# Performance work log

Hardware: AMD Instinct MI355X
Metric: run time of the kernel (lower is better)

Reference implementation:

```python
import jax, jax.numpy as jnp
import numpy as np

C = 256  # in_channels
B, N = 8, 2048


def setup_inputs() -> dict:
    key = jax.random.key(0)
    ks = jax.random.split(key, 9)
    s = 1.0 / np.sqrt(C)  # conv1d default init scale (approx)
    return {
        "x": jax.random.normal(ks[0], (B, C, N), jnp.float32),
        "wq": jax.random.normal(ks[1], (C, C), jnp.float32) * s,
        "bq": jax.random.normal(ks[2], (C,), jnp.float32) * s,
        "wk": jax.random.normal(ks[3], (C, C), jnp.float32) * s,
        "bk": jax.random.normal(ks[4], (C,), jnp.float32) * s,
        "wv": jax.random.normal(ks[5], (C, C), jnp.float32) * s,
        "bv": jax.random.normal(ks[6], (C,), jnp.float32) * s,
        "wo": jax.random.normal(ks[7], (C, C), jnp.float32) * s,
        "bo": jax.random.normal(ks[8], (C,), jnp.float32) * s,
    }


def reference(x, wq, bq, wk, bk, wv, bv, wo, bo):
    # 1x1 Conv1d == channel-wise linear: [C_out,C_in] x [B,C_in,N] -> [B,C_out,N]
    proj = lambda w, b, t: jnp.einsum('ci,bin->bcn', w, t) + b[None, :, None]
    q = proj(wq, bq, x)
    k = proj(wk, bk, x)
    v = proj(wv, bv, x)
    norm = 1.0 / (x.shape[1] ** 0.5)
    # scores: w[b,n,m] = sum_c q[b,c,n] k[b,c,m]
    w = jnp.einsum('bcn,bcm->bnm', q, k) * norm
    w = jax.nn.softmax(w, axis=2)
    # attn output: sum_m v[b,c,m] w[b,n,m] -> [B,C,N]
    av = jnp.einsum('bcm,bnm->bcn', v, w)
    out = proj(wo, bo, av)
    return x + out
```

## Files before the change

kernel.cpp:

```cpp
#include <hip/hip_runtime.h>
#include <hip/hip_bf16.h>

#define CCH 256
#define NSEQ 2048
#define BATCH 8

typedef __hip_bfloat16 bf16;
typedef short s8v __attribute__((ext_vector_type(8)));
typedef float f4v __attribute__((ext_vector_type(4)));
typedef float f16v __attribute__((ext_vector_type(16)));

struct __align__(8) bf16x4 { bf16 v[4]; };

__device__ __forceinline__ float b2f(bf16 h) { return __bfloat162float(h); }
__device__ __forceinline__ bf16 f2b(float f) { return __float2bfloat16(f); }

#define MFMA16(a, b, c) __builtin_amdgcn_mfma_f32_16x16x32_bf16((a), (b), (c), 0, 0, 0)
#define MFMA32(a, b, c) __builtin_amdgcn_mfma_f32_32x32x16_bf16((a), (b), (c), 0, 0, 0)

__device__ __forceinline__ void gload_lds16(const bf16* g, bf16* l) {
    __builtin_amdgcn_global_load_lds(
        (const __attribute__((address_space(1))) unsigned int*)(g),
        (__attribute__((address_space(3))) unsigned int*)(l), 16, 0, 0);
}

__global__ __launch_bounds__(256) void prepw_kernel(
    const float* __restrict__ wq, const float* __restrict__ wk,
    const float* __restrict__ wv,
    bf16* __restrict__ wqb, bf16* __restrict__ wkb, bf16* __restrict__ wvb)
{
    int base = (blockIdx.x * 256 + threadIdx.x) * 8;
    int mat = base >> 16, off = base & 65535;
    const float* s = (mat == 0) ? wq : (mat == 1) ? wk : wv;
    bf16* d       = (mat == 0) ? wqb : (mat == 1) ? wkb : wvb;
    int doff = off ^ (((off >> 8) & 7) << 3);
    bf16 tmp[8];
    #pragma unroll
    for (int j = 0; j < 8; ++j) tmp[j] = f2b(s[off + j]);
    *(s8v*)&d[doff] = *(const s8v*)tmp;
}

__global__ __launch_bounds__(512, 4) void qkvprep_kernel(
    const float* __restrict__ x,
    const bf16* __restrict__ Wq, const bf16* __restrict__ Wk,
    const bf16* __restrict__ Wv,
    const float* __restrict__ bq, const float* __restrict__ bk,
    const float* __restrict__ bv,
    bf16* __restrict__ qTt, bf16* __restrict__ kTt, bf16* __restrict__ Vt)
{
    __shared__ bf16 xs[64][260];
    __shared__ bf16 wbuf[2][2][4096];

    const int tile = blockIdx.x;
    const int flat0 = tile * 64;
    const int phase = blockIdx.y;
    const int b = flat0 >> 11, nn = flat0 & 2047;
    const int tid = threadIdx.x;
    const int w = tid >> 6, lane = tid & 63;
    const int l15 = lane & 15, quad = lane >> 4;
    const int ng = w & 3;
    const int ch = w >> 2;
    const float* xb = x + (size_t)b * CCH * NSEQ;

    bf16* qt = qTt + (size_t)tile * 16384;
    bf16* kt = kTt + (size_t)tile * 16384;
    bf16* Vtb = Vt + (size_t)b * CCH * NSEQ;

    auto chunk_ptr = [&](int j) -> const bf16* {
        if (phase == 0)
            return (j < 8) ? Wq + (size_t)(ch * 8 + j) * 4096
                           : Wk + (size_t)(ch * 4 + (j - 8)) * 4096;
        else
            return (j < 8) ? Wv + (size_t)(ch * 8 + j) * 4096
                           : Wk + (size_t)(8 + ch * 4 + (j - 8)) * 4096;
    };
    auto stage = [&](int j, int par) {
        const bf16* src = chunk_ptr(j);
        bf16* dst = &wbuf[ch][par][0];
        int seg = (w & 3) * 2;
        gload_lds16(src + (seg + 0) * 512 + lane * 8, dst + (seg + 0) * 512);
        gload_lds16(src + (seg + 1) * 512 + lane * 8, dst + (seg + 1) * 512);
    };

    stage(0, 0);
    #pragma unroll
    for (int i = 0; i < 8; ++i) {
        int f4i = i * 512 + tid;
        int c = f4i >> 4, nq = f4i & 15;
        float4 v4 = *(const float4*)&xb[(size_t)c * NSEQ + nn + nq * 4];
        xs[nq * 4 + 0][c] = f2b(v4.x);
        xs[nq * 4 + 1][c] = f2b(v4.y);
        xs[nq * 4 + 2][c] = f2b(v4.z);
        xs[nq * 4 + 3][c] = f2b(v4.w);
    }
    __syncthreads();

    s8v xf[8];
    #pragma unroll
    for (int t = 0; t < 8; ++t)
        xf[t] = *(const s8v*)&xs[ng * 16 + l15][t * 32 + quad * 8];

    int par = 0;
    #pragma unroll
    for (int j = 0; j < 12; ++j) {
        if (j < 11) stage(j + 1, par ^ 1);

        const char* wb = (const char*)&wbuf[ch][par][0];
        s8v wf[8];
        #pragma unroll
        for (int t = 0; t < 8; ++t)
            wf[t] = *(const s8v*)(wb + l15 * 512 +
                                  ((t * 64 + quad * 16) ^ ((l15 & 7) << 4)));

        if (phase == 0 || j >= 8) {
            f4v a0 = {}, a1 = {};
            #pragma unroll
            for (int t = 0; t < 4; ++t) {
                a0 = MFMA16(wf[t], xf[t], a0);
                a1 = MFMA16(wf[t + 4], xf[t + 4], a1);
            }
            const bool isq = (phase == 0) && (j < 8);
            const int cs = (phase == 0)
                ? (j < 8 ? ch * 8 + j : ch * 4 + (j - 8))
                : (8 + ch * 4 + (j - 8));
            const float* bm = isq ? bq : bk;
            bf16* ot = isq ? qt : kt;
            const float sc = isq ? 0.0625f : 1.0f;
            float4 bb4 = *(const float4*)&bm[cs * 16 + quad * 4];
            float bbr[4] = { bb4.x, bb4.y, bb4.z, bb4.w };
            bf16x4 pk;
            #pragma unroll
            for (int r = 0; r < 4; ++r)
                pk.v[r] = f2b((a0[r] + a1[r] + bbr[r]) * sc);
            int nl = ng * 16 + l15;
            *(bf16x4*)&ot[(cs * 2 + (quad >> 1)) * 512 + nl * 8 + (quad & 1) * 4] = pk;
        } else {
            f4v a0 = {}, a1 = {};
            #pragma unroll
            for (int t = 0; t < 4; ++t) {
                a0 = MFMA16(xf[t], wf[t], a0);
                a1 = MFMA16(xf[t + 4], wf[t + 4], a1);
            }
            const int cs = ch * 8 + j;
            int c = cs * 16 + l15;
            float bb = bv[c];
            int nb0 = nn + ng * 16 + quad * 4;
            bf16x4 pk;
            #pragma unroll
            for (int r = 0; r < 4; ++r)
                pk.v[r] = f2b(a0[r] + a1[r] + bb);
            *(bf16x4*)&Vtb[(size_t)(nb0 >> 5) * 8192 + (size_t)c * 32 + (nb0 & 31)] = pk;
        }
        __syncthreads();
        par ^= 1;
    }
}

__global__ __launch_bounds__(256, 2) void flash_kernel(
    const bf16* __restrict__ qTt, const bf16* __restrict__ kTt,
    const bf16* __restrict__ Vt, bf16* __restrict__ Opart,
    float* __restrict__ lpart)
{
    __shared__ bf16 Kc[16384];
    __shared__ bf16 Ps[64][68];
    __shared__ float l_s[2][64];

    const int b = blockIdx.x, nt = blockIdx.y, ms = blockIdx.z;
    const int tid = threadIdx.x;
    const int W = tid >> 6, lane = tid & 63;
    const int l31 = lane & 31, h = lane >> 5;
    const int ng = W >> 1, mg = W & 1;
    const int mb = ms * 16;
    const bf16* Vtb = Vt + (size_t)b * CCH * NSEQ;

    s8v qf[16];
    {
        const bf16* qt = qTt + (size_t)(b * 32 + nt) * 16384;
        #pragma unroll
        for (int t = 0; t < 16; ++t)
            qf[t] = *(const s8v*)&qt[(t * 2 + h) * 512 + (ng * 32 + l31) * 8];
    }
    const bf16* vrow[2];
    #pragma unroll
    for (int cr = 0; cr < 2; ++cr)
        vrow[cr] = Vtb + (size_t)(W * 64 + cr * 32 + l31) * 32 + h * 8;

    f16v O[2][2] = {};
    float lacc[16] = {};

    {
        const bf16* kt = kTt + (size_t)(b * 32 + mb) * 16384;
        #pragma unroll
        for (int i = 0; i < 8; ++i) {
            int ch = W * 8 + i;
            gload_lds16(kt + ch * 512 + lane * 8, &Kc[ch * 512]);
        }
    }
    __syncthreads();

    for (int mt = 0; mt < 16; ++mt) {
        f16v S0 = {}, S1 = {};
        #pragma unroll
        for (int t = 0; t < 8; ++t) {
            s8v kf0 = *(const s8v*)&Kc[(t * 2 + h) * 512 + (mg * 32 + l31) * 8];
            s8v kf1 = *(const s8v*)&Kc[((t + 8) * 2 + h) * 512 + (mg * 32 + l31) * 8];
            S0 = MFMA32(qf[t], kf0, S0);
            S1 = MFMA32(qf[t + 8], kf1, S1);
        }
        s8v vf[2][4];
        #pragma unroll
        for (int ks = 0; ks < 4; ++ks)
            #pragma unroll
            for (int cr = 0; cr < 2; ++cr)
                vf[cr][ks] = *(const s8v*)(vrow[cr]
                    + (size_t)((mb + mt) * 2 + (ks >> 1)) * 8192
                    + (ks & 1) * 16);
        #pragma unroll
        for (int reg = 0; reg < 16; ++reg) {
            float e = __expf(fminf(S0[reg] + S1[reg], 60.f));
            lacc[reg] += e;
            int row = (reg & 3) + 8 * (reg >> 2) + 4 * h;
            Ps[ng * 32 + row][mg * 32 + l31] = f2b(e);
        }
        __syncthreads();

        if (mt < 15) {
            const bf16* kt = kTt + (size_t)(b * 32 + mb + mt + 1) * 16384;
            #pragma unroll
            for (int i = 0; i < 8; ++i) {
                int ch = W * 8 + i;
                gload_lds16(kt + ch * 512 + lane * 8, &Kc[ch * 512]);
            }
        }
        #pragma unroll
        for (int ks = 0; ks < 4; ++ks) {
            s8v pf0 = *(const s8v*)&Ps[l31][ks * 16 + h * 8];
            s8v pf1 = *(const s8v*)&Ps[32 + l31][ks * 16 + h * 8];
            O[0][0] = MFMA32(vf[0][ks], pf0, O[0][0]);
            O[0][1] = MFMA32(vf[0][ks], pf1, O[0][1]);
            O[1][0] = MFMA32(vf[1][ks], pf0, O[1][0]);
            O[1][1] = MFMA32(vf[1][ks], pf1, O[1][1]);
        }
        __syncthreads();
    }

    #pragma unroll
    for (int reg = 0; reg < 16; ++reg) {
        float s = lacc[reg];
        #pragma unroll
        for (int off = 1; off < 32; off <<= 1) s += __shfl_xor(s, off);
        lacc[reg] = s;
    }
    if (l31 == 0) {
        #pragma unroll
        for (int reg = 0; reg < 16; ++reg) {
            int row = (reg & 3) + 8 * (reg >> 2) + 4 * h;
            l_s[mg][ng * 32 + row] = lacc[reg];
        }
    }
    __syncthreads();
    const size_t pb = (size_t)(b * 32 + nt) * 2 + ms;
    if (tid < 64) lpart[pb * 64 + tid] = l_s[0][tid] + l_s[1][tid];

    bf16* Ob = Opart + pb * 16384;
    #pragma unroll
    for (int cr = 0; cr < 2; ++cr)
        #pragma unroll
        for (int g2 = 0; g2 < 2; ++g2) {
            int n = g2 * 32 + l31;
            #pragma unroll
            for (int q2 = 0; q2 < 4; ++q2) {
                bf16x4 pk;
                #pragma unroll
                for (int j = 0; j < 4; ++j) pk.v[j] = f2b(O[cr][g2][q2 * 4 + j]);
                int c = W * 64 + cr * 32 + q2 * 8 + 4 * h;
                *(bf16x4*)&Ob[(size_t)n * 256 + c] = pk;
            }
        }
}

__global__ __launch_bounds__(256, 2) void outproj_kernel(
    const bf16* __restrict__ Opart, const float* __restrict__ lpart,
    const float* __restrict__ Wo, const float* __restrict__ bo,
    const float* __restrict__ x, float* __restrict__ out)
{
    __shared__ bf16 avs[64][260];
    __shared__ float ils[64];

    const int bx = blockIdx.x;
    const int flat0 = bx * 64;
    const int c0 = blockIdx.y * 128;
    const int tid = threadIdx.x;
    const int w = tid >> 6, lane = tid & 63;
    const int l15 = lane & 15, quad = lane >> 4;

    if (tid < 64)
        ils[tid] = 1.f / (lpart[(size_t)(bx * 2) * 64 + tid]
                        + lpart[(size_t)(bx * 2 + 1) * 64 + tid]);
    __syncthreads();

    const bf16x4* O0 = (const bf16x4*)(Opart + (size_t)(bx * 2) * 16384);
    const bf16x4* O1 = O0 + 4096;
    #pragma unroll
    for (int i = 0; i < 16; ++i) {
        int u = i * 256 + tid;
        int n = u >> 6;
        bf16x4 a = O0[u], bb = O1[u];
        float il = ils[n];
        bf16x4 o;
        #pragma unroll
        for (int t = 0; t < 4; ++t)
            o.v[t] = f2b((b2f(a.v[t]) + b2f(bb.v[t])) * il);
        *(bf16x4*)&avs[n][(u & 63) * 4] = o;
    }
    __syncthreads();

    const int bidx = flat0 >> 11, nn = flat0 & 2047;
    const size_t base = (size_t)bidx * CCH * NSEQ;

    for (int g = 0; g < 2; ++g) {
        const int cg = c0 + g * 64 + w * 16;
        s8v af[8];
        #pragma unroll
        for (int t = 0; t < 8; ++t) {
            const float* wp = Wo + (size_t)(cg + l15) * CCH + t * 32 + quad * 8;
            float4 f0 = *(const float4*)wp;
            float4 f1 = *(const float4*)(wp + 4);
            bf16 a8[8] = { f2b(f0.x), f2b(f0.y), f2b(f0.z), f2b(f0.w),
                           f2b(f1.x), f2b(f1.y), f2b(f1.z), f2b(f1.w) };
            af[t] = *(const s8v*)a8;
        }
        f4v O[4] = {};
        #pragma unroll
        for (int nt = 0; nt < 4; ++nt)
            #pragma unroll
            for (int t = 0; t < 8; ++t) {
                s8v br = *(const s8v*)&avs[nt * 16 + l15][t * 32 + quad * 8];
                O[nt] = MFMA16(af[t], br, O[nt]);
            }
        #pragma unroll
        for (int r = 0; r < 4; ++r) {
            int c = cg + quad * 4 + r;
            float bb = bo[c];
            #pragma unroll
            for (int nt = 0; nt < 4; ++nt) {
                size_t idx = base + (size_t)c * NSEQ + nn + nt * 16 + l15;
                out[idx] = O[nt][r] + bb + x[idx];
            }
        }
    }
}

extern "C" void kernel_launch(void* const* d_in, const int* in_sizes, int n_in,
                              void* d_out, int out_size, void* d_ws, size_t ws_size,
                              hipStream_t stream) {
    (void)in_sizes; (void)n_in; (void)out_size; (void)ws_size;
    const float* x  = (const float*)d_in[0];
    const float* wq = (const float*)d_in[1];
    const float* bq = (const float*)d_in[2];
    const float* wk = (const float*)d_in[3];
    const float* bk = (const float*)d_in[4];
    const float* wv = (const float*)d_in[5];
    const float* bv = (const float*)d_in[6];
    const float* wo = (const float*)d_in[7];
    const float* bo = (const float*)d_in[8];
    float* out = (float*)d_out;

    const size_t T = (size_t)BATCH * CCH * NSEQ;
    bf16* qTt  = (bf16*)d_ws;
    bf16* kTt  = qTt + T;
    bf16* Vt   = kTt + T;
    bf16* wqb  = Vt + T;
    bf16* wkb  = wqb + 65536;
    bf16* wvb  = wkb + 65536;
    float* lpart = (float*)(wvb + 65536);
    bf16* Opart  = (bf16*)(lpart + 32768);

    prepw_kernel<<<96, 256, 0, stream>>>(wq, wk, wv, wqb, wkb, wvb);
    qkvprep_kernel<<<dim3(256, 2), 512, 0, stream>>>(
        x, wqb, wkb, wvb, bq, bk, bv, qTt, kTt, Vt);
    flash_kernel<<<dim3(8, 32, 2), 256, 0, stream>>>(qTt, kTt, Vt, Opart, lpart);
    outproj_kernel<<<dim3(256, 2), 256, 0, stream>>>(Opart, lpart, wo, bo, x, out);
}
```

Measured before the change: 162.6 us.

## Split flash attention key range three ways and relayout V tiles

The key/value sequence is now split into three partitions instead of two, so the grid grows from 512 to 768 blocks. The launch bound rises to 3 blocks per CU to improve occupancy and load balance on the device. V is stored in a new 16-column tiled layout that matches the flash kernel's per-tile loads, and MFMA sections are wrapped in s_setprio raises. The output projection now merges three partial results, which adds extra partial-buffer traffic and may put register pressure on the kernel under the tighter launch bound.

After: 262.9 us. +61.7%, slower.

```diff
diff --git a/kernel.cpp b/kernel.cpp
--- a/kernel.cpp
+++ b/kernel.cpp
@@ -144,19 +144,20 @@
             const int cs = ch * 8 + j;
             int c = cs * 16 + l15;
             float bb = bv[c];
-            int nb0 = nn + ng * 16 + quad * 4;
             bf16x4 pk;
             #pragma unroll
             for (int r = 0; r < 4; ++r)
                 pk.v[r] = f2b(a0[r] + a1[r] + bb);
-            *(bf16x4*)&Vtb[(size_t)(nb0 >> 5) * 8192 + (size_t)c * 32 + (nb0 & 31)] = pk;
+            const int m16 = (nn >> 4) + ng;
+            size_t e0 = ((size_t)m16 * 256 + c) * 16 + (quad >> 1) * 8 + (quad & 1) * 4;
+            *(bf16x4*)&Vtb[e0] = pk;
         }
         __syncthreads();
         par ^= 1;
     }
 }
 
-__global__ __launch_bounds__(256, 2) void flash_kernel(
+__global__ __launch_bounds__(256, 3) void flash_kernel(
     const bf16* __restrict__ qTt, const bf16* __restrict__ kTt,
     const bf16* __restrict__ Vt, bf16* __restrict__ Opart,
     float* __restrict__ lpart)
@@ -170,7 +171,7 @@
     const int W = tid >> 6, lane = tid & 63;
     const int l31 = lane & 31, h = lane >> 5;
     const int ng = W >> 1, mg = W & 1;
-    const int mb = ms * 16;
+    const int a0 = (ms * 32) / 3, a1 = ((ms + 1) * 32) / 3;
     const bf16* Vtb = Vt + (size_t)b * CCH * NSEQ;
 
     s8v qf[16];
@@ -180,16 +181,13 @@
         for (int t = 0; t < 16; ++t)
             qf[t] = *(const s8v*)&qt[(t * 2 + h) * 512 + (ng * 32 + l31) * 8];
     }
-    const bf16* vrow[2];
-    #pragma unroll
-    for (int cr = 0; cr < 2; ++cr)
-        vrow[cr] = Vtb + (size_t)(W * 64 + cr * 32 + l31) * 32 + h * 8;
+    const bf16* vbase = Vtb + (size_t)(W * 64 + l31) * 16 + h * 8;
 
     f16v O[2][2] = {};
     float lacc[16] = {};
 
     {
-        const bf16* kt = kTt + (size_t)(b * 32 + mb) * 16384;
+        const bf16* kt = kTt + (size_t)(b * 32 + a0) * 16384;
         #pragma unroll
         for (int i = 0; i < 8; ++i) {
             int ch = W * 8 + i;
@@ -198,8 +196,9 @@
     }
     __syncthreads();
 
-    for (int mt = 0; mt < 16; ++mt) {
+    for (int a = a0; a < a1; ++a) {
         f16v S0 = {}, S1 = {};
+        __builtin_amdgcn_s_setprio(1);
         #pragma unroll
         for (int t = 0; t < 8; ++t) {
             s8v kf0 = *(const s8v*)&Kc[(t * 2 + h) * 512 + (mg * 32 + l31) * 8];
@@ -207,14 +206,14 @@
             S0 = MFMA32(qf[t], kf0, S0);
             S1 = MFMA32(qf[t + 8], kf1, S1);
         }
+        __builtin_amdgcn_s_setprio(0);
         s8v vf[2][4];
         #pragma unroll
         for (int ks = 0; ks < 4; ++ks)
             #pragma unroll
             for (int cr = 0; cr < 2; ++cr)
-                vf[cr][ks] = *(const s8v*)(vrow[cr]
-                    + (size_t)((mb + mt) * 2 + (ks >> 1)) * 8192
-                    + (ks & 1) * 16);
+                vf[cr][ks] = *(const s8v*)(vbase + (size_t)(a * 4 + ks) * 4096
+                                           + cr * 512);
         #pragma unroll
         for (int reg = 0; reg < 16; ++reg) {
             float e = __expf(fminf(S0[reg] + S1[reg], 60.f));
@@ -224,14 +223,15 @@
         }
         __syncthreads();
 
-        if (mt < 15) {
-            const bf16* kt = kTt + (size_t)(b * 32 + mb + mt + 1) * 16384;
+        if (a + 1 < a1) {
+            const bf16* kt = kTt + (size_t)(b * 32 + a + 1) * 16384;
             #pragma unroll
             for (int i = 0; i < 8; ++i) {
                 int ch = W * 8 + i;
                 gload_lds16(kt + ch * 512 + lane * 8, &Kc[ch * 512]);
             }
         }
+        __builtin_amdgcn_s_setprio(1);
         #pragma unroll
         for (int ks = 0; ks < 4; ++ks) {
             s8v pf0 = *(const s8v*)&Ps[l31][ks * 16 + h * 8];
@@ -241,6 +241,7 @@
             O[1][0] = MFMA32(vf[1][ks], pf0, O[1][0]);
             O[1][1] = MFMA32(vf[1][ks], pf1, O[1][1]);
         }
+        __builtin_amdgcn_s_setprio(0);
         __syncthreads();
     }
 
@@ -259,7 +260,7 @@
         }
     }
     __syncthreads();
-    const size_t pb = (size_t)(b * 32 + nt) * 2 + ms;
+    const size_t pb = (size_t)(b * 32 + nt) * 3 + ms;
     if (tid < 64) lpart[pb * 64 + tid] = l_s[0][tid] + l_s[1][tid];
 
     bf16* Ob = Opart + pb * 16384;
@@ -295,22 +296,24 @@
     const int l15 = lane & 15, quad = lane >> 4;
 
     if (tid < 64)
-        ils[tid] = 1.f / (lpart[(size_t)(bx * 2) * 64 + tid]
-                        + lpart[(size_t)(bx * 2 + 1) * 64 + tid]);
-    __syncthreads();
-
-    const bf16x4* O0 = (const bf16x4*)(Opart + (size_t)(bx * 2) * 16384);
+        ils[tid] = 1.f / (lpart[(size_t)(bx * 3) * 64 + tid]
+                        + lpart[(size_t)(bx * 3 + 1) * 64 + tid]
+                        + lpart[(size_t)(bx * 3 + 2) * 64 + tid]);
+    __syncthreads();
+
+    const bf16x4* O0 = (const bf16x4*)(Opart + (size_t)(bx * 3) * 16384);
     const bf16x4* O1 = O0 + 4096;
+    const bf16x4* O2 = O1 + 4096;
     #pragma unroll
     for (int i = 0; i < 16; ++i) {
         int u = i * 256 + tid;
         int n = u >> 6;
-        bf16x4 a = O0[u], bb = O1[u];
+        bf16x4 a = O0[u], bb = O1[u], cc = O2[u];
         float il = ils[n];
         bf16x4 o;
         #pragma unroll
         for (int t = 0; t < 4; ++t)
-            o.v[t] = f2b((b2f(a.v[t]) + b2f(bb.v[t])) * il);
+            o.v[t] = f2b((b2f(a.v[t]) + b2f(bb.v[t]) + b2f(cc.v[t])) * il);
         *(bf16x4*)&avs[n][(u & 63) * 4] = o;
     }
     __syncthreads();
@@ -374,11 +377,11 @@
     bf16* wkb  = wqb + 65536;
     bf16* wvb  = wkb + 65536;
     float* lpart = (float*)(wvb + 65536);
-    bf16* Opart  = (bf16*)(lpart + 32768);
+    bf16* Opart  = (bf16*)(lpart + 768 * 64);
 
     prepw_kernel<<<96, 256, 0, stream>>>(wq, wk, wv, wqb, wkb, wvb);
     qkvprep_kernel<<<dim3(256, 2), 512, 0, stream>>>(
         x, wqb, wkb, wvb, bq, bk, bv, qTt, kTt, Vt);
-    flash_kernel<<<dim3(8, 32, 2), 256, 0, stream>>>(qTt, kTt, Vt, Opart, lpart);
+    flash_kernel<<<dim3(8, 32, 3), 256, 0, stream>>>(qTt, kTt, Vt, Opart, lpart);
     outproj_kernel<<<dim3(256, 2), 256, 0, stream>>>(Opart, lpart, wo, bo, x, out);
 }
```

## Double-buffer K tiles in LDS, retile V layout, add MFMA priority hints

Applied to the files above, without the earlier changes.

K tiles are now double-buffered in LDS, and the next tile's async load is issued at the start of each iteration so it overlaps the QK^T MFMAs. The projection kernel writes V in a new 16-row blocked layout, which gives contiguous per-lane loads in the flash kernel. s_setprio brackets around the MFMA sections are meant to favor the matrix work when waves are scheduled. LDS use grows by 32KB, which may reduce occupancy relative to the launch bound of 2 blocks per CU.

Result: no change. 163.5 us (+0.5%).

```diff
diff --git a/kernel.cpp b/kernel.cpp
--- a/kernel.cpp
+++ b/kernel.cpp
@@ -144,12 +144,13 @@
             const int cs = ch * 8 + j;
             int c = cs * 16 + l15;
             float bb = bv[c];
-            int nb0 = nn + ng * 16 + quad * 4;
             bf16x4 pk;
             #pragma unroll
             for (int r = 0; r < 4; ++r)
                 pk.v[r] = f2b(a0[r] + a1[r] + bb);
-            *(bf16x4*)&Vtb[(size_t)(nb0 >> 5) * 8192 + (size_t)c * 32 + (nb0 & 31)] = pk;
+            const int m16 = (nn >> 4) + ng;
+            size_t e0 = ((size_t)m16 * 256 + c) * 16 + (quad >> 1) * 8 + (quad & 1) * 4;
+            *(bf16x4*)&Vtb[e0] = pk;
         }
         __syncthreads();
         par ^= 1;
@@ -161,7 +162,7 @@
     const bf16* __restrict__ Vt, bf16* __restrict__ Opart,
     float* __restrict__ lpart)
 {
-    __shared__ bf16 Kc[16384];
+    __shared__ bf16 Kc[2][16384];
     __shared__ bf16 Ps[64][68];
     __shared__ float l_s[2][64];
 
@@ -180,41 +181,44 @@
         for (int t = 0; t < 16; ++t)
             qf[t] = *(const s8v*)&qt[(t * 2 + h) * 512 + (ng * 32 + l31) * 8];
     }
-    const bf16* vrow[2];
-    #pragma unroll
-    for (int cr = 0; cr < 2; ++cr)
-        vrow[cr] = Vtb + (size_t)(W * 64 + cr * 32 + l31) * 32 + h * 8;
+    const bf16* vbase = Vtb + (size_t)(W * 64 + l31) * 16 + h * 8;
 
     f16v O[2][2] = {};
     float lacc[16] = {};
 
-    {
-        const bf16* kt = kTt + (size_t)(b * 32 + mb) * 16384;
+    auto stageK = [&](int a, int buf) {
+        const bf16* kt = kTt + (size_t)(b * 32 + a) * 16384;
         #pragma unroll
         for (int i = 0; i < 8; ++i) {
             int ch = W * 8 + i;
-            gload_lds16(kt + ch * 512 + lane * 8, &Kc[ch * 512]);
-        }
-    }
+            gload_lds16(kt + ch * 512 + lane * 8, &Kc[buf][ch * 512]);
+        }
+    };
+
+    stageK(mb, 0);
     __syncthreads();
 
     for (int mt = 0; mt < 16; ++mt) {
+        const int cur = mt & 1;
+        if (mt < 15) stageK(mb + mt + 1, cur ^ 1);
+
         f16v S0 = {}, S1 = {};
+        __builtin_amdgcn_s_setprio(1);
         #pragma unroll
         for (int t = 0; t < 8; ++t) {
-            s8v kf0 = *(const s8v*)&Kc[(t * 2 + h) * 512 + (mg * 32 + l31) * 8];
-            s8v kf1 = *(const s8v*)&Kc[((t + 8) * 2 + h) * 512 + (mg * 32 + l31) * 8];
+            s8v kf0 = *(const s8v*)&Kc[cur][(t * 2 + h) * 512 + (mg * 32 + l31) * 8];
+            s8v kf1 = *(const s8v*)&Kc[cur][((t + 8) * 2 + h) * 512 + (mg * 32 + l31) * 8];
             S0 = MFMA32(qf[t], kf0, S0);
             S1 = MFMA32(qf[t + 8], kf1, S1);
         }
+        __builtin_amdgcn_s_setprio(0);
         s8v vf[2][4];
         #pragma unroll
         for (int ks = 0; ks < 4; ++ks)
             #pragma unroll
             for (int cr = 0; cr < 2; ++cr)
-                vf[cr][ks] = *(const s8v*)(vrow[cr]
-                    + (size_t)((mb + mt) * 2 + (ks >> 1)) * 8192
-                    + (ks & 1) * 16);
+                vf[cr][ks] = *(const s8v*)(vbase
+                    + (size_t)((mb + mt) * 4 + ks) * 4096 + cr * 512);
         #pragma unroll
         for (int reg = 0; reg < 16; ++reg) {
             float e = __expf(fminf(S0[reg] + S1[reg], 60.f));
@@ -224,14 +228,7 @@
         }
         __syncthreads();
 
-        if (mt < 15) {
-            const bf16* kt = kTt + (size_t)(b * 32 + mb + mt + 1) * 16384;
-            #pragma unroll
-            for (int i = 0; i < 8; ++i) {
-                int ch = W * 8 + i;
-                gload_lds16(kt + ch * 512 + lane * 8, &Kc[ch * 512]);
-            }
-        }
+        __builtin_amdgcn_s_setprio(1);
         #pragma unroll
         for (int ks = 0; ks < 4; ++ks) {
             s8v pf0 = *(const s8v*)&Ps[l31][ks * 16 + h * 8];
@@ -241,6 +238,7 @@
             O[1][0] = MFMA32(vf[1][ks], pf0, O[1][0]);
             O[1][1] = MFMA32(vf[1][ks], pf1, O[1][1]);
         }
+        __builtin_amdgcn_s_setprio(0);
         __syncthreads();
     }
 
```
